# Optimization experiments

Hardware: AMD Instinct MI355X
Metric: run time of the kernel (lower is better)

## Reference

```python
import jax, jax.numpy as jnp
import numpy as np

B, S, H, I, E, K = 4, 2048, 1024, 4096, 8, 2


def setup_inputs() -> dict:
    key = jax.random.key(0)
    ks = jax.random.split(key, 5)
    scale = 1.0 / np.sqrt(H)
    return {
        "hidden_states": jax.random.normal(ks[0], (B, S, H), dtype=jnp.float32),
        "router_w": jax.random.normal(ks[1], (E, H), dtype=jnp.float32) * scale,
        "gate_w": jax.random.normal(ks[2], (E, I, H), dtype=jnp.float32) * scale,
        "up_w": jax.random.normal(ks[3], (E, I, H), dtype=jnp.float32) * scale,
        "down_w": jax.random.normal(ks[4], (E, H, I), dtype=jnp.float32) * (1.0 / np.sqrt(I)),
        "top_k": K,
    }


def reference(hidden_states, router_w, gate_w, up_w, down_w, top_k):
    # Router: logits -> softmax -> top-k -> renormalized weights (eval mode, no jitter)
    logits = jnp.einsum("bsh,eh->bse", hidden_states, router_w)
    probs = jax.nn.softmax(logits, axis=-1)
    expert_weights, expert_indices = jax.lax.top_k(probs, top_k)  # [B,S,K]
    expert_weights = expert_weights / expert_weights.sum(axis=-1, keepdims=True)

    n_experts = router_w.shape[0]
    # Per-token combine weight for each expert: [B,S,E]
    combine = (jax.nn.one_hot(expert_indices, n_experts, dtype=expert_weights.dtype)
               * expert_weights[..., None]).sum(axis=-2)

    out = jnp.zeros_like(hidden_states)
    for e in range(n_experts):  # fixed small expert count
        g = jax.nn.silu(hidden_states @ gate_w[e].T)  # [B,S,I]
        u = hidden_states @ up_w[e].T                 # [B,S,I]
        y = (g * u) @ down_w[e].T                     # [B,S,H]
        out = out + combine[..., e:e + 1] * y
    return out
```

## Files before the change

### kernel.cpp

```cpp
#include <hip/hip_runtime.h>
#include <hip/hip_bf16.h>
#include <math.h>
#include <stdint.h>

#define TOKENS 8192
#define HD 1024
#define ID 4096
#define NE 8
#define RMAX 18432
#define MAXT 72

typedef __attribute__((ext_vector_type(8))) short short8v;
typedef __attribute__((ext_vector_type(4))) float f32x4;

typedef const __attribute__((address_space(1))) unsigned int* gas_u32p;
typedef __attribute__((address_space(3))) unsigned int* las_u32p;

__device__ __forceinline__ void stage16(const void* g, void* l) {
  __builtin_amdgcn_global_load_lds((gas_u32p)g, (las_u32p)l, 16, 0, 0);
}

#define BARRIER asm volatile("s_barrier" ::: "memory")
#define WAITLGKM asm volatile("s_waitcnt lgkmcnt(0)" ::: "memory")
#define VMC0 asm volatile("s_waitcnt vmcnt(0)" ::: "memory")
#define VMC2 asm volatile("s_waitcnt vmcnt(2)" ::: "memory")
#define VMC6 asm volatile("s_waitcnt vmcnt(6)" ::: "memory")
#define VMC8 asm volatile("s_waitcnt vmcnt(8)" ::: "memory")

__global__ __launch_bounds__(256) void convert3_kernel(
    const float* __restrict__ s0, const float* __restrict__ s1, const float* __restrict__ s2,
    __hip_bfloat16* __restrict__ d0) {
  int r = blockIdx.x >> 14;
  const float* src = (r == 0) ? s0 : ((r == 1) ? s1 : s2);
  __hip_bfloat16* dst = d0 + (size_t)r * ((size_t)NE * ID * HD);
  size_t i = (((size_t)(blockIdx.x & 16383)) * 256 + threadIdx.x) * 8;
  float4 a = ((const float4*)(src + i))[0];
  float4 b = ((const float4*)(src + i))[1];
  union { __hip_bfloat16 h[8]; int4 v; } u;
  u.h[0] = __float2bfloat16(a.x); u.h[1] = __float2bfloat16(a.y);
  u.h[2] = __float2bfloat16(a.z); u.h[3] = __float2bfloat16(a.w);
  u.h[4] = __float2bfloat16(b.x); u.h[5] = __float2bfloat16(b.y);
  u.h[6] = __float2bfloat16(b.z); u.h[7] = __float2bfloat16(b.w);
  *(int4*)(dst + i) = u.v;
}

__global__ __launch_bounds__(256) void router_kernel(
    const float* __restrict__ h, const float* __restrict__ rw,
    __hip_bfloat16* __restrict__ hx, int* __restrict__ tidx,
    float* __restrict__ tw, int* __restrict__ cnt) {
  int wid = threadIdx.x >> 6, lane = threadIdx.x & 63;
  int t = blockIdx.x * 4 + wid;
  const float4* h4 = (const float4*)(h + (size_t)t * HD);
  float x[16];
  {
    float4 xa = h4[lane * 4 + 0], xb = h4[lane * 4 + 1], xc = h4[lane * 4 + 2], xd = h4[lane * 4 + 3];
    x[0] = xa.x; x[1] = xa.y; x[2] = xa.z; x[3] = xa.w;
    x[4] = xb.x; x[5] = xb.y; x[6] = xb.z; x[7] = xb.w;
    x[8] = xc.x; x[9] = xc.y; x[10] = xc.z; x[11] = xc.w;
    x[12] = xd.x; x[13] = xd.y; x[14] = xd.z; x[15] = xd.w;
  }
  union { __hip_bfloat16 hb[16]; int4 v[2]; } u;
#pragma unroll
  for (int j = 0; j < 16; j++) u.hb[j] = __float2bfloat16(x[j]);
  {
    int4* hxp = (int4*)(hx + (size_t)t * HD + lane * 16);
    hxp[0] = u.v[0]; hxp[1] = u.v[1];
  }
  double acc[NE];
#pragma unroll
  for (int e = 0; e < NE; e++) {
    const float4* w4 = (const float4*)(rw + e * HD);
    float4 wa = w4[lane * 4 + 0], wb = w4[lane * 4 + 1], wc = w4[lane * 4 + 2], wd = w4[lane * 4 + 3];
    double s = 0.0;
    s += (double)x[0] * wa.x + (double)x[1] * wa.y + (double)x[2] * wa.z + (double)x[3] * wa.w;
    s += (double)x[4] * wb.x + (double)x[5] * wb.y + (double)x[6] * wb.z + (double)x[7] * wb.w;
    s += (double)x[8] * wc.x + (double)x[9] * wc.y + (double)x[10] * wc.z + (double)x[11] * wc.w;
    s += (double)x[12] * wd.x + (double)x[13] * wd.y + (double)x[14] * wd.z + (double)x[15] * wd.w;
    acc[e] = s;
  }
#pragma unroll
  for (int off = 32; off >= 1; off >>= 1)
#pragma unroll
    for (int e = 0; e < NE; e++) acc[e] += __shfl_xor(acc[e], off, 64);
  if (lane == 0) {
    int i0 = 0; double l0 = acc[0];
#pragma unroll
    for (int e = 1; e < NE; e++) if (acc[e] > l0) { l0 = acc[e]; i0 = e; }
    int i1 = -1; double l1 = -1.0e300;
#pragma unroll
    for (int e = 0; e < NE; e++) if (e != i0 && acc[e] > l1) { l1 = acc[e]; i1 = e; }
    double r = exp(l1 - l0);
    float w0 = (float)(1.0 / (1.0 + r));
    float w1 = (float)(r / (1.0 + r));
    tidx[t * 2 + 0] = i0; tidx[t * 2 + 1] = i1;
    tw[t * 2 + 0] = w0;  tw[t * 2 + 1] = w1;
    atomicAdd(&cnt[i0], 1); atomicAdd(&cnt[i1], 1);
  }
}

__global__ void scan_kernel(const int* __restrict__ cnt, int* __restrict__ ofs, int* __restrict__ cnt2) {
  if (threadIdx.x == 0) {
    int a = 0;
    for (int e = 0; e < NE; e++) { ofs[e] = a; a += (cnt[e] + 255) & ~255; }
    ofs[NE] = a;
  }
  if (threadIdx.x < NE) cnt2[threadIdx.x] = 0;
}

__global__ __launch_bounds__(256) void scatter_kernel(
    const int* __restrict__ tidx, const float* __restrict__ tw,
    const int* __restrict__ ofs, int* __restrict__ cnt2,
    int* __restrict__ rowmap, int* __restrict__ slots) {
  int t = blockIdx.x * 256 + threadIdx.x;
#pragma unroll
  for (int k = 0; k < 2; k++) {
    int e = tidx[t * 2 + k];
    int pos = atomicAdd(&cnt2[e], 1);
    int row = ofs[e] + pos;
    rowmap[row] = t;
    slots[t * 2 + k] = row;
  }
}

#define MFMA44(ACC, AF, BF)                                                                \
  { _Pragma("unroll") for (int m_ = 0; m_ < 4; m_++)                                       \
    _Pragma("unroll") for (int n_ = 0; n_ < 4; n_++)                                       \
    _Pragma("unroll") for (int k_ = 0; k_ < 2; k_++)                                       \
      ACC[m_][n_] = __builtin_amdgcn_mfma_f32_16x16x32_bf16(                               \
          AF[m_][k_], BF[n_][k_], ACC[m_][n_], 0, 0, 0); }

__global__ __launch_bounds__(512, 2) void gemm1_kernel(
    const __hip_bfloat16* __restrict__ hx, const __hip_bfloat16* __restrict__ Wg,
    const __hip_bfloat16* __restrict__ Wu, const int* __restrict__ rowmap,
    const int* __restrict__ ofs, const __hip_bfloat16* __restrict__ zrow,
    __hip_bfloat16* __restrict__ act) {
  __shared__ __align__(128) char lds[131072];
  const int nwg = gridDim.x;
  int wg0 = blockIdx.x;
  int wg = (wg0 & 7) * (nwg >> 3) + (wg0 >> 3);
  const int tm = wg >> 5, tn = wg & 31;
  const int Rtot = ofs[NE];
  const int row0 = tm * 256;
  if (row0 >= Rtot) return;
  int e = 0;
#pragma unroll
  for (int i = 1; i < NE; i++) e += (row0 >= ofs[i]);
  const int tid = threadIdx.x, wid = tid >> 6, lane = tid & 63;
  const int wm = wid >> 1, wn = wid & 1;
  const int fr = lane & 15, fkE = (lane >> 4) << 3;
  const int wmB = wm * 64, wnB = wn * 64;

  const char* srcA[4]; const char* srcG[2]; const char* srcU[2];
  int ldA[4], ldG[2], ldU[2];
#pragma unroll
  for (int j = 0; j < 4; j++) {
    int d = j * 8192 + tid * 16;
    int row = d >> 7;
    int kb = (d ^ (((d >> 7) & 7) << 4)) & 127;
    int tok = rowmap[row0 + row];
    const __hip_bfloat16* base = (tok >= 0) ? (hx + (size_t)tok * HD) : zrow;
    srcA[j] = (const char*)base + kb;
    ldA[j] = j * 8192 + wid * 1024;
  }
#pragma unroll
  for (int j = 0; j < 2; j++) {
    int d = j * 8192 + tid * 16;
    int row = d >> 7;
    int kb = (d ^ (((d >> 7) & 7) << 4)) & 127;
    srcG[j] = (const char*)(Wg + ((size_t)e * ID + tn * 128 + row) * HD) + kb;
    srcU[j] = (const char*)(Wu + ((size_t)e * ID + tn * 128 + row) * HD) + kb;
    ldG[j] = 32768 + j * 8192 + wid * 1024;
    ldU[j] = 49152 + j * 8192 + wid * 1024;
  }
#define STG_A(j, t, bf) stage16(srcA[j] + (size_t)(t) * 128, (char*)lds + (bf) * 65536 + ldA[j])
#define STG_G(j, t, bf) stage16(srcG[j] + (size_t)(t) * 128, (char*)lds + (bf) * 65536 + ldG[j])
#define STG_U(j, t, bf) stage16(srcU[j] + (size_t)(t) * 128, (char*)lds + (bf) * 65536 + ldU[j])

  auto RD = [&](int bf, int poff, int rowi, int kki) -> short8v {
    int o = ((rowi + fr) << 7) + ((kki << 5) + fkE) * 2;
    o ^= ((o >> 7) & 7) << 4;
    return *(const short8v*)(&lds[bf * 65536 + poff + o]);
  };

  f32x4 accG[4][4], accU[4][4];
#pragma unroll
  for (int m = 0; m < 4; m++)
#pragma unroll
    for (int n = 0; n < 4; n++) { accG[m][n] = (f32x4)(0.0f); accU[m][n] = (f32x4)(0.0f); }

  const int NT = HD / 64;
#pragma unroll
  for (int j = 0; j < 4; j++) STG_A(j, 0, 0);
  STG_G(0, 0, 0); STG_G(1, 0, 0);
  STG_U(0, 0, 0); STG_U(1, 0, 0);
#pragma unroll
  for (int j = 0; j < 4; j++) STG_A(j, 1, 1);
  STG_G(0, 1, 1); STG_G(1, 1, 1);
  VMC8; BARRIER;

#pragma unroll 1
  for (int I = 0; I < NT / 2; ++I) {
    const int t0 = 2 * I;
    const bool more = (t0 + 2 < NT);
    short8v a[4][2], b[4][2];
#pragma unroll
    for (int m = 0; m < 4; m++) { a[m][0] = RD(0, 0, wmB + m * 16, 0); a[m][1] = RD(0, 0, wmB + m * 16, 1); }
#pragma unroll
    for (int n = 0; n < 4; n++) { b[n][0] = RD(0, 32768, wnB + n * 16, 0); b[n][1] = RD(0, 32768, wnB + n * 16, 1); }
    STG_U(0, t0 + 1, 1); STG_U(1, t0 + 1, 1);
    BARRIER; WAITLGKM;
    __builtin_amdgcn_s_setprio(1); MFMA44(accG, a, b); __builtin_amdgcn_s_setprio(0);
    VMC8; BARRIER;
#pragma unroll
    for (int n = 0; n < 4; n++) { b[n][0] = RD(0, 49152, wnB + n * 16, 0); b[n][1] = RD(0, 49152, wnB + n * 16, 1); }
    if (more) {
      STG_A(0, t0 + 2, 0); STG_A(1, t0 + 2, 0); STG_A(2, t0 + 2, 0); STG_A(3, t0 + 2, 0);
      STG_G(0, t0 + 2, 0); STG_G(1, t0 + 2, 0);
    }
    BARRIER; WAITLGKM;
    __builtin_amdgcn_s_setprio(1); MFMA44(accU, a, b); __builtin_amdgcn_s_setprio(0);
    if (more) { VMC8; } else { VMC2; }
    BARRIER;
#pragma unroll
    for (int m = 0; m < 4; m++) { a[m][0] = RD(1, 0, wmB + m * 16, 0); a[m][1] = RD(1, 0, wmB + m * 16, 1); }
#pragma unroll
    for (int n = 0; n < 4; n++) { b[n][0] = RD(1, 32768, wnB + n * 16, 0); b[n][1] = RD(1, 32768, wnB + n * 16, 1); }
    if (more) { STG_U(0, t0 + 2, 0); STG_U(1, t0 + 2, 0); }
    BARRIER; WAITLGKM;
    __builtin_amdgcn_s_setprio(1); MFMA44(accG, a, b); __builtin_amdgcn_s_setprio(0);
    if (more) { VMC8; } else { VMC0; }
    BARRIER;
#pragma unroll
    for (int n = 0; n < 4; n++) { b[n][0] = RD(1, 49152, wnB + n * 16, 0); b[n][1] = RD(1, 49152, wnB + n * 16, 1); }
    if (more) {
      STG_A(0, t0 + 3, 1); STG_A(1, t0 + 3, 1); STG_A(2, t0 + 3, 1); STG_A(3, t0 + 3, 1);
      STG_G(0, t0 + 3, 1); STG_G(1, t0 + 3, 1);
    }
    BARRIER; WAITLGKM;
    __builtin_amdgcn_s_setprio(1); MFMA44(accU, a, b); __builtin_amdgcn_s_setprio(0);
    if (more) { VMC8; } else { VMC0; }
    BARRIER;
  }
#undef STG_A
#undef STG_G
#undef STG_U

  const int rb = row0 + wmB + ((lane >> 4) << 2);
  const int cb = tn * 128 + wnB + fr;
#pragma unroll
  for (int m = 0; m < 4; m++)
#pragma unroll
    for (int i = 0; i < 4; i++) {
      int r = rb + m * 16 + i;
      __hip_bfloat16* dst = act + (size_t)r * ID + cb;
#pragma unroll
      for (int n = 0; n < 4; n++) {
        float g = accG[m][n][i], uu = accU[m][n][i];
        float s = g / (1.0f + __expf(-g));
        dst[n * 16] = __float2bfloat16(s * uu);
      }
    }
}

__global__ __launch_bounds__(512, 2) void gemm2_kernel(
    const __hip_bfloat16* __restrict__ act, const __hip_bfloat16* __restrict__ Wd,
    const int* __restrict__ ofs, float* __restrict__ ybuf) {
  __shared__ __align__(128) char lds[147456];
  const int nwg = gridDim.x;
  int wg0 = blockIdx.x;
  int wg = (wg0 & 7) * (nwg >> 3) + (wg0 >> 3);
  const int tm = wg >> 3, tn = wg & 7;
  const int Rtot = ofs[NE];
  const int row0 = tm * 256;
  if (row0 >= Rtot) return;
  int e = 0;
#pragma unroll
  for (int i = 1; i < NE; i++) e += (row0 >= ofs[i]);
  const int tid = threadIdx.x, wid = tid >> 6, lane = tid & 63;
  const int wm = wid >> 1, wn = wid & 1;
  const int fr = lane & 15, fkE = (lane >> 4) << 3;
  const int wmB = wm * 64, wnB = wn * 64;

  const char* srcA[4]; const char* srcB[2];
  int ldA[4], ldB[2];
#pragma unroll
  for (int j = 0; j < 4; j++) {
    int d = j * 8192 + tid * 16;
    int row = d >> 7;
    int kb = (d ^ (((d >> 7) & 7) << 4)) & 127;
    srcA[j] = (const char*)(act + (size_t)(row0 + row) * ID) + kb;
    ldA[j] = j * 8192 + wid * 1024;
  }
#pragma unroll
  for (int j = 0; j < 2; j++) {
    int d = j * 8192 + tid * 16;
    int row = d >> 7;
    int kb = (d ^ (((d >> 7) & 7) << 4)) & 127;
    srcB[j] = (const char*)(Wd + ((size_t)e * HD + tn * 128 + row) * ID) + kb;
    ldB[j] = 32768 + j * 8192 + wid * 1024;
  }
#define STG_A2(j, t, q) stage16(srcA[j] + (size_t)(t) * 128, (char*)lds + (q) * 49152 + ldA[j])
#define STG_B2(j, t, q) stage16(srcB[j] + (size_t)(t) * 128, (char*)lds + (q) * 49152 + ldB[j])

  auto RD = [&](const char* base, int poff, int rowi, int kki) -> short8v {
    int o = ((rowi + fr) << 7) + ((kki << 5) + fkE) * 2;
    o ^= ((o >> 7) & 7) << 4;
    return *(const short8v*)(base + poff + o);
  };

  f32x4 acc[4][4];
#pragma unroll
  for (int m = 0; m < 4; m++)
#pragma unroll
    for (int n = 0; n < 4; n++) acc[m][n] = (f32x4)(0.0f);

  const int NT = ID / 64;
#pragma unroll
  for (int j = 0; j < 4; j++) STG_A2(j, 0, 0);
  STG_B2(0, 0, 0); STG_B2(1, 0, 0);
#pragma unroll
  for (int j = 0; j < 4; j++) STG_A2(j, 1, 1);
  STG_B2(0, 1, 1); STG_B2(1, 1, 1);
  VMC6; BARRIER;

  int bq = 0;
#pragma unroll 1
  for (int T = 0; T < NT; ++T) {
    const bool more = (T + 2 < NT);
    int sq = (bq >= 1) ? (bq - 1) : 2;
    const char* base = (const char*)lds + bq * 49152;
    short8v a[4][2], b[4][2];
#pragma unroll
    for (int m = 0; m < 4; m++) { a[m][0] = RD(base, 0, wmB + m * 16, 0); a[m][1] = RD(base, 0, wmB + m * 16, 1); }
#pragma unroll
    for (int n = 0; n < 4; n++) { b[n][0] = RD(base, 32768, wnB + n * 16, 0); b[n][1] = RD(base, 32768, wnB + n * 16, 1); }
    if (more) {
      STG_A2(0, T + 2, sq); STG_A2(1, T + 2, sq); STG_A2(2, T + 2, sq); STG_A2(3, T + 2, sq);
      STG_B2(0, T + 2, sq); STG_B2(1, T + 2, sq);
    }
    BARRIER; WAITLGKM;
    __builtin_amdgcn_s_setprio(1); MFMA44(acc, a, b); __builtin_amdgcn_s_setprio(0);
    if (more) { VMC6; } else { VMC0; }
    BARRIER;
    bq = (bq == 2) ? 0 : (bq + 1);
  }
#undef STG_A2
#undef STG_B2

  const int rb = row0 + wmB + ((lane >> 4) << 2);
  const int cb = tn * 128 + wnB + fr;
#pragma unroll
  for (int m = 0; m < 4; m++)
#pragma unroll
    for (int i = 0; i < 4; i++) {
      int r = rb + m * 16 + i;
      float* dst = ybuf + (size_t)r * HD + cb;
#pragma unroll
      for (int n = 0; n < 4; n++) dst[n * 16] = acc[m][n][i];
    }
}

__global__ __launch_bounds__(256) void combine_kernel(
    const float* __restrict__ ybuf, const int* __restrict__ slots,
    const float* __restrict__ tw, float* __restrict__ out) {
  int t = blockIdx.x * 4 + (threadIdx.x >> 6);
  int lane = threadIdx.x & 63;
  int r0 = slots[t * 2 + 0], r1 = slots[t * 2 + 1];
  float w0 = tw[t * 2 + 0], w1 = tw[t * 2 + 1];
  const float4* y0 = (const float4*)(ybuf + (size_t)r0 * HD);
  const float4* y1 = (const float4*)(ybuf + (size_t)r1 * HD);
  float4* o = (float4*)(out + (size_t)t * HD);
#pragma unroll
  for (int j = 0; j < 4; j++) {
    int ix = j * 64 + lane;
    float4 a = y0[ix], b = y1[ix];
    float4 c;
    c.x = w0 * a.x + w1 * b.x; c.y = w0 * a.y + w1 * b.y;
    c.z = w0 * a.z + w1 * b.z; c.w = w0 * a.w + w1 * b.w;
    o[ix] = c;
  }
}

extern "C" void kernel_launch(void* const* d_in, const int* in_sizes, int n_in,
                              void* d_out, int out_size, void* d_ws, size_t ws_size,
                              hipStream_t stream) {
  (void)in_sizes; (void)n_in; (void)out_size; (void)ws_size;
  const float* h  = (const float*)d_in[0];
  const float* rw = (const float*)d_in[1];
  const float* gw = (const float*)d_in[2];
  const float* uw = (const float*)d_in[3];
  const float* dw = (const float*)d_in[4];
  float* out = (float*)d_out;

  char* ws = (char*)d_ws;
  size_t off = 0;
  auto alloc = [&](size_t bytes) { char* p = ws + off; off += (bytes + 255) & ~255ULL; return p; };
  __hip_bfloat16* wg  = (__hip_bfloat16*)alloc((size_t)NE * ID * HD * 2);
  __hip_bfloat16* wu  = (__hip_bfloat16*)alloc((size_t)NE * ID * HD * 2);
  __hip_bfloat16* wd  = (__hip_bfloat16*)alloc((size_t)NE * HD * ID * 2);
  __hip_bfloat16* act = (__hip_bfloat16*)alloc((size_t)RMAX * ID * 2);
  __hip_bfloat16* hx  = (__hip_bfloat16*)alloc((size_t)TOKENS * HD * 2);
  float* ybuf = (float*)alloc((size_t)RMAX * HD * 4);
  __hip_bfloat16* zrow = (__hip_bfloat16*)alloc(HD * 2);
  int* rowmap = (int*)alloc(RMAX * 4);
  int* tidx   = (int*)alloc(TOKENS * 2 * 4);
  float* twt  = (float*)alloc(TOKENS * 2 * 4);
  int* slots  = (int*)alloc(TOKENS * 2 * 4);
  int* cnt    = (int*)alloc(256);
  int* cnt2   = (int*)alloc(256);
  int* ofs    = (int*)alloc(256);

  hipMemsetAsync(cnt, 0, NE * 4, stream);
  hipMemsetAsync(rowmap, 0xFF, RMAX * 4, stream);
  hipMemsetAsync(zrow, 0, HD * 2, stream);

  convert3_kernel<<<49152, 256, 0, stream>>>(gw, uw, dw, wg);
  router_kernel<<<TOKENS / 4, 256, 0, stream>>>(h, rw, hx, tidx, twt, cnt);
  scan_kernel<<<1, 64, 0, stream>>>(cnt, ofs, cnt2);
  scatter_kernel<<<TOKENS / 256, 256, 0, stream>>>(tidx, twt, ofs, cnt2, rowmap, slots);
  gemm1_kernel<<<MAXT * 32, 512, 0, stream>>>(hx, wg, wu, rowmap, ofs, zrow, act);
  gemm2_kernel<<<MAXT * 8, 512, 0, stream>>>(act, wd, ofs, ybuf);
  combine_kernel<<<TOKENS / 4, 256, 0, stream>>>(ybuf, slots, twt, out);
}
```

Baseline: 919.2 us.

## Enlarge GEMM warp tiles to 128x64, fuse combine into gemm2 via atomics

Both expert GEMMs move to a 4x2 wave layout where each wave computes a 128x64 tile over an 8-phase K loop. Gemm1 stacks the gate and up weights into one 256-wide B tile and pairs the G and U halves through LDS in the epilogue. Gemm2 widens its N tile to 256 and scatters weighted results directly into the output with float atomics, which removes the ybuf round trip and the combine kernel. This costs a memset of the output, atomic contention on each token's two expert rows, and more accumulator registers per wave.

Result: slower. 1.097 ms (+19.3%).

```diff
diff --git a/kernel.cpp b/kernel.cpp
--- a/kernel.cpp
+++ b/kernel.cpp
@@ -23,9 +23,7 @@
 #define BARRIER asm volatile("s_barrier" ::: "memory")
 #define WAITLGKM asm volatile("s_waitcnt lgkmcnt(0)" ::: "memory")
 #define VMC0 asm volatile("s_waitcnt vmcnt(0)" ::: "memory")
-#define VMC2 asm volatile("s_waitcnt vmcnt(2)" ::: "memory")
-#define VMC6 asm volatile("s_waitcnt vmcnt(6)" ::: "memory")
-#define VMC8 asm volatile("s_waitcnt vmcnt(8)" ::: "memory")
+#define VMC4 asm volatile("s_waitcnt vmcnt(4)" ::: "memory")
 
 __global__ __launch_bounds__(256) void convert3_kernel(
     const float* __restrict__ s0, const float* __restrict__ s1, const float* __restrict__ s2,
@@ -110,7 +108,7 @@
 __global__ __launch_bounds__(256) void scatter_kernel(
     const int* __restrict__ tidx, const float* __restrict__ tw,
     const int* __restrict__ ofs, int* __restrict__ cnt2,
-    int* __restrict__ rowmap, int* __restrict__ slots) {
+    int* __restrict__ rowmap, float* __restrict__ wrow) {
   int t = blockIdx.x * 256 + threadIdx.x;
 #pragma unroll
   for (int k = 0; k < 2; k++) {
@@ -118,16 +116,77 @@
     int pos = atomicAdd(&cnt2[e], 1);
     int row = ofs[e] + pos;
     rowmap[row] = t;
-    slots[t * 2 + k] = row;
-  }
-}
-
-#define MFMA44(ACC, AF, BF)                                                                \
+    wrow[row] = tw[t * 2 + k];
+  }
+}
+
+#define MFMA16(ACC, MO, AF, BF)                                                            \
   { _Pragma("unroll") for (int m_ = 0; m_ < 4; m_++)                                       \
     _Pragma("unroll") for (int n_ = 0; n_ < 4; n_++)                                       \
-    _Pragma("unroll") for (int k_ = 0; k_ < 2; k_++)                                       \
-      ACC[m_][n_] = __builtin_amdgcn_mfma_f32_16x16x32_bf16(                               \
-          AF[m_][k_], BF[n_][k_], ACC[m_][n_], 0, 0, 0); }
+      ACC[(MO) + m_][n_] = __builtin_amdgcn_mfma_f32_16x16x32_bf16(                        \
+          AF[m_], BF[n_], ACC[(MO) + m_][n_], 0, 0, 0); }
+
+#define KLOOP_8PHASE(NT)                                                                   \
+  _Pragma("unroll 1")                                                                      \
+  for (int I = 0; I < (NT) / 2; ++I) {                                                     \
+    const int t0 = 2 * I;                                                                  \
+    const bool more = (t0 + 2 < (NT));                                                     \
+    short8v a0[4], a1[4], b0[4], b1[4];                                                    \
+                                                                                   \
+    _Pragma("unroll") for (int m = 0; m < 4; m++) a0[m] = RD(0, 0, wmB + m * 16, 0);       \
+    _Pragma("unroll") for (int n = 0; n < 4; n++) b0[n] = RD(0, 32768, wnB + n * 16, 0);   \
+    STG_A(0, t0 + 1, 1); STG_A(1, t0 + 1, 1);                                              \
+    BARRIER; WAITLGKM;                                                                     \
+    __builtin_amdgcn_s_setprio(1); MFMA16(acc, 0, a0, b0); __builtin_amdgcn_s_setprio(0);  \
+    BARRIER;                                                                               \
+                                                                                   \
+    _Pragma("unroll") for (int m = 0; m < 4; m++) a1[m] = RD(0, 0, wmB + m * 16, 1);       \
+    _Pragma("unroll") for (int n = 0; n < 4; n++) b1[n] = RD(0, 32768, wnB + n * 16, 1);   \
+    STG_A(2, t0 + 1, 1); STG_A(3, t0 + 1, 1);                                              \
+    BARRIER; WAITLGKM;                                                                     \
+    __builtin_amdgcn_s_setprio(1); MFMA16(acc, 0, a1, b1); __builtin_amdgcn_s_setprio(0);  \
+    BARRIER;                                                                               \
+                                                                                   \
+    _Pragma("unroll") for (int m = 0; m < 4; m++) a0[m] = RD(0, 0, wmB + 64 + m * 16, 0);  \
+    if (more) { STG_B(0, t0 + 2, 0); STG_B(1, t0 + 2, 0); }                                \
+    BARRIER; WAITLGKM;                                                                     \
+    __builtin_amdgcn_s_setprio(1); MFMA16(acc, 4, a0, b0); __builtin_amdgcn_s_setprio(0);  \
+    BARRIER;                                                                               \
+                                                                                   \
+    _Pragma("unroll") for (int m = 0; m < 4; m++) a1[m] = RD(0, 0, wmB + 64 + m * 16, 1);  \
+    if (more) { STG_B(2, t0 + 2, 0); STG_B(3, t0 + 2, 0); }                                \
+    BARRIER; WAITLGKM;                                                                     \
+    __builtin_amdgcn_s_setprio(1); MFMA16(acc, 4, a1, b1); __builtin_amdgcn_s_setprio(0);  \
+    if (more) { VMC4; } else { VMC0; }                                                     \
+    BARRIER;                                                                               \
+                                                                                   \
+    _Pragma("unroll") for (int m = 0; m < 4; m++) a0[m] = RD(1, 0, wmB + m * 16, 0);       \
+    _Pragma("unroll") for (int n = 0; n < 4; n++) b0[n] = RD(1, 32768, wnB + n * 16, 0);   \
+    if (more) { STG_A(0, t0 + 2, 0); STG_A(1, t0 + 2, 0); }                                \
+    BARRIER; WAITLGKM;                                                                     \
+    __builtin_amdgcn_s_setprio(1); MFMA16(acc, 0, a0, b0); __builtin_amdgcn_s_setprio(0);  \
+    BARRIER;                                                                               \
+                                                                                   \
+    _Pragma("unroll") for (int m = 0; m < 4; m++) a1[m] = RD(1, 0, wmB + m * 16, 1);       \
+    _Pragma("unroll") for (int n = 0; n < 4; n++) b1[n] = RD(1, 32768, wnB + n * 16, 1);   \
+    if (more) { STG_A(2, t0 + 2, 0); STG_A(3, t0 + 2, 0); }                                \
+    BARRIER; WAITLGKM;                                                                     \
+    __builtin_amdgcn_s_setprio(1); MFMA16(acc, 0, a1, b1); __builtin_amdgcn_s_setprio(0);  \
+    BARRIER;                                                                               \
+                                                                                   \
+    _Pragma("unroll") for (int m = 0; m < 4; m++) a0[m] = RD(1, 0, wmB + 64 + m * 16, 0);  \
+    if (more) { STG_B(0, t0 + 3, 1); STG_B(1, t0 + 3, 1); }                                \
+    BARRIER; WAITLGKM;                                                                     \
+    __builtin_amdgcn_s_setprio(1); MFMA16(acc, 4, a0, b0); __builtin_amdgcn_s_setprio(0);  \
+    BARRIER;                                                                               \
+                                                                                   \
+    _Pragma("unroll") for (int m = 0; m < 4; m++) a1[m] = RD(1, 0, wmB + 64 + m * 16, 1);  \
+    if (more) { STG_B(2, t0 + 3, 1); STG_B(3, t0 + 3, 1); }                                \
+    BARRIER; WAITLGKM;                                                                     \
+    __builtin_amdgcn_s_setprio(1); MFMA16(acc, 4, a1, b1); __builtin_amdgcn_s_setprio(0);  \
+    if (more) { VMC4; } else { VMC0; }                                                     \
+    BARRIER;                                                                               \
+  }
 
 __global__ __launch_bounds__(512, 2) void gemm1_kernel(
     const __hip_bfloat16* __restrict__ hx, const __hip_bfloat16* __restrict__ Wg,
@@ -146,35 +205,29 @@
 #pragma unroll
   for (int i = 1; i < NE; i++) e += (row0 >= ofs[i]);
   const int tid = threadIdx.x, wid = tid >> 6, lane = tid & 63;
-  const int wm = wid >> 1, wn = wid & 1;
+  const int wm = wid >> 2, wn = wid & 3;
   const int fr = lane & 15, fkE = (lane >> 4) << 3;
-  const int wmB = wm * 64, wnB = wn * 64;
-
-  const char* srcA[4]; const char* srcG[2]; const char* srcU[2];
-  int ldA[4], ldG[2], ldU[2];
+  const int wmB = wm * 128, wnB = wn * 64;
+
+  const char* srcA[4]; const char* srcB[4];
+  int ldA[4], ldB[4];
 #pragma unroll
   for (int j = 0; j < 4; j++) {
     int d = j * 8192 + tid * 16;
     int row = d >> 7;
     int kb = (d ^ (((d >> 7) & 7) << 4)) & 127;
     int tok = rowmap[row0 + row];
-    const __hip_bfloat16* base = (tok >= 0) ? (hx + (size_t)tok * HD) : zrow;
-    srcA[j] = (const char*)base + kb;
+    const __hip_bfloat16* abase = (tok >= 0) ? (hx + (size_t)tok * HD) : zrow;
+    srcA[j] = (const char*)abase + kb;
     ldA[j] = j * 8192 + wid * 1024;
-  }
-#pragma unroll
-  for (int j = 0; j < 2; j++) {
-    int d = j * 8192 + tid * 16;
-    int row = d >> 7;
-    int kb = (d ^ (((d >> 7) & 7) << 4)) & 127;
-    srcG[j] = (const char*)(Wg + ((size_t)e * ID + tn * 128 + row) * HD) + kb;
-    srcU[j] = (const char*)(Wu + ((size_t)e * ID + tn * 128 + row) * HD) + kb;
-    ldG[j] = 32768 + j * 8192 + wid * 1024;
-    ldU[j] = 49152 + j * 8192 + wid * 1024;
+    const __hip_bfloat16* wbase = (row < 128)
+        ? (Wg + ((size_t)e * ID + tn * 128 + row) * HD)
+        : (Wu + ((size_t)e * ID + tn * 128 + (row - 128)) * HD);
+    srcB[j] = (const char*)wbase + kb;
+    ldB[j] = 32768 + j * 8192 + wid * 1024;
   }
 #define STG_A(j, t, bf) stage16(srcA[j] + (size_t)(t) * 128, (char*)lds + (bf) * 65536 + ldA[j])
-#define STG_G(j, t, bf) stage16(srcG[j] + (size_t)(t) * 128, (char*)lds + (bf) * 65536 + ldG[j])
-#define STG_U(j, t, bf) stage16(srcU[j] + (size_t)(t) * 128, (char*)lds + (bf) * 65536 + ldU[j])
+#define STG_B(j, t, bf) stage16(srcB[j] + (size_t)(t) * 128, (char*)lds + (bf) * 65536 + ldB[j])
 
   auto RD = [&](int bf, int poff, int rowi, int kki) -> short8v {
     int o = ((rowi + fr) << 7) + ((kki << 5) + fkE) * 2;
@@ -182,94 +235,62 @@
     return *(const short8v*)(&lds[bf * 65536 + poff + o]);
   };
 
-  f32x4 accG[4][4], accU[4][4];
+  f32x4 acc[8][4];
+#pragma unroll
+  for (int m = 0; m < 8; m++)
+#pragma unroll
+    for (int n = 0; n < 4; n++) acc[m][n] = (f32x4)(0.0f);
+
+  const int NT = HD / 64;
+#pragma unroll
+  for (int j = 0; j < 4; j++) STG_A(j, 0, 0);
+#pragma unroll
+  for (int j = 0; j < 4; j++) STG_B(j, 0, 0);
+#pragma unroll
+  for (int j = 0; j < 4; j++) STG_B(j, 1, 1);
+  VMC4; BARRIER;
+
+  KLOOP_8PHASE(NT)
+#undef STG_A
+#undef STG_B
+
+  const bool isG = (wn < 2);
+  float* xslot = (float*)(lds + wid * 16384);
+  const float* pslot = (const float*)(lds + (wid ^ 2) * 16384);
 #pragma unroll
   for (int m = 0; m < 4; m++)
 #pragma unroll
-    for (int n = 0; n < 4; n++) { accG[m][n] = (f32x4)(0.0f); accU[m][n] = (f32x4)(0.0f); }
-
-  const int NT = HD / 64;
-#pragma unroll
-  for (int j = 0; j < 4; j++) STG_A(j, 0, 0);
-  STG_G(0, 0, 0); STG_G(1, 0, 0);
-  STG_U(0, 0, 0); STG_U(1, 0, 0);
-#pragma unroll
-  for (int j = 0; j < 4; j++) STG_A(j, 1, 1);
-  STG_G(0, 1, 1); STG_G(1, 1, 1);
-  VMC8; BARRIER;
-
-#pragma unroll 1
-  for (int I = 0; I < NT / 2; ++I) {
-    const int t0 = 2 * I;
-    const bool more = (t0 + 2 < NT);
-    short8v a[4][2], b[4][2];
-#pragma unroll
-    for (int m = 0; m < 4; m++) { a[m][0] = RD(0, 0, wmB + m * 16, 0); a[m][1] = RD(0, 0, wmB + m * 16, 1); }
-#pragma unroll
-    for (int n = 0; n < 4; n++) { b[n][0] = RD(0, 32768, wnB + n * 16, 0); b[n][1] = RD(0, 32768, wnB + n * 16, 1); }
-    STG_U(0, t0 + 1, 1); STG_U(1, t0 + 1, 1);
-    BARRIER; WAITLGKM;
-    __builtin_amdgcn_s_setprio(1); MFMA44(accG, a, b); __builtin_amdgcn_s_setprio(0);
-    VMC8; BARRIER;
-#pragma unroll
-    for (int n = 0; n < 4; n++) { b[n][0] = RD(0, 49152, wnB + n * 16, 0); b[n][1] = RD(0, 49152, wnB + n * 16, 1); }
-    if (more) {
-      STG_A(0, t0 + 2, 0); STG_A(1, t0 + 2, 0); STG_A(2, t0 + 2, 0); STG_A(3, t0 + 2, 0);
-      STG_G(0, t0 + 2, 0); STG_G(1, t0 + 2, 0);
-    }
-    BARRIER; WAITLGKM;
-    __builtin_amdgcn_s_setprio(1); MFMA44(accU, a, b); __builtin_amdgcn_s_setprio(0);
-    if (more) { VMC8; } else { VMC2; }
-    BARRIER;
-#pragma unroll
-    for (int m = 0; m < 4; m++) { a[m][0] = RD(1, 0, wmB + m * 16, 0); a[m][1] = RD(1, 0, wmB + m * 16, 1); }
-#pragma unroll
-    for (int n = 0; n < 4; n++) { b[n][0] = RD(1, 32768, wnB + n * 16, 0); b[n][1] = RD(1, 32768, wnB + n * 16, 1); }
-    if (more) { STG_U(0, t0 + 2, 0); STG_U(1, t0 + 2, 0); }
-    BARRIER; WAITLGKM;
-    __builtin_amdgcn_s_setprio(1); MFMA44(accG, a, b); __builtin_amdgcn_s_setprio(0);
-    if (more) { VMC8; } else { VMC0; }
-    BARRIER;
-#pragma unroll
-    for (int n = 0; n < 4; n++) { b[n][0] = RD(1, 49152, wnB + n * 16, 0); b[n][1] = RD(1, 49152, wnB + n * 16, 1); }
-    if (more) {
-      STG_A(0, t0 + 3, 1); STG_A(1, t0 + 3, 1); STG_A(2, t0 + 3, 1); STG_A(3, t0 + 3, 1);
-      STG_G(0, t0 + 3, 1); STG_G(1, t0 + 3, 1);
-    }
-    BARRIER; WAITLGKM;
-    __builtin_amdgcn_s_setprio(1); MFMA44(accU, a, b); __builtin_amdgcn_s_setprio(0);
-    if (more) { VMC8; } else { VMC0; }
-    BARRIER;
-  }
-#undef STG_A
-#undef STG_G
-#undef STG_U
-
-  const int rb = row0 + wmB + ((lane >> 4) << 2);
-  const int cb = tn * 128 + wnB + fr;
+    for (int n = 0; n < 4; n++)
+      *(f32x4*)(xslot + (size_t)(m * 4 + n) * 256 + lane * 4) = acc[isG ? 4 + m : m][n];
+  __syncthreads();
+  const int g4 = (lane >> 4) << 2;
+  const int colb = tn * 128 + (wn & 1) * 64 + fr;
+  const int rb = row0 + wmB + (isG ? 0 : 64) + g4;
 #pragma unroll
   for (int m = 0; m < 4; m++)
 #pragma unroll
-    for (int i = 0; i < 4; i++) {
-      int r = rb + m * 16 + i;
-      __hip_bfloat16* dst = act + (size_t)r * ID + cb;
-#pragma unroll
-      for (int n = 0; n < 4; n++) {
-        float g = accG[m][n][i], uu = accU[m][n][i];
+    for (int n = 0; n < 4; n++) {
+      f32x4 other = *(const f32x4*)(pslot + (size_t)(m * 4 + n) * 256 + lane * 4);
+      f32x4 own = acc[isG ? m : 4 + m][n];
+#pragma unroll
+      for (int i = 0; i < 4; i++) {
+        float g = isG ? own[i] : other[i];
+        float u = isG ? other[i] : own[i];
         float s = g / (1.0f + __expf(-g));
-        dst[n * 16] = __float2bfloat16(s * uu);
+        act[(size_t)(rb + m * 16 + i) * ID + colb + n * 16] = __float2bfloat16(s * u);
       }
     }
 }
 
 __global__ __launch_bounds__(512, 2) void gemm2_kernel(
     const __hip_bfloat16* __restrict__ act, const __hip_bfloat16* __restrict__ Wd,
-    const int* __restrict__ ofs, float* __restrict__ ybuf) {
-  __shared__ __align__(128) char lds[147456];
+    const int* __restrict__ rowmap, const float* __restrict__ wrow,
+    const int* __restrict__ ofs, float* __restrict__ out) {
+  __shared__ __align__(128) char lds[131072];
   const int nwg = gridDim.x;
   int wg0 = blockIdx.x;
   int wg = (wg0 & 7) * (nwg >> 3) + (wg0 >> 3);
-  const int tm = wg >> 3, tn = wg & 7;
+  const int tm = wg >> 2, tn = wg & 3;
   const int Rtot = ofs[NE];
   const int row0 = tm * 256;
   if (row0 >= Rtot) return;
@@ -277,12 +298,12 @@
 #pragma unroll
   for (int i = 1; i < NE; i++) e += (row0 >= ofs[i]);
   const int tid = threadIdx.x, wid = tid >> 6, lane = tid & 63;
-  const int wm = wid >> 1, wn = wid & 1;
+  const int wm = wid >> 2, wn = wid & 3;
   const int fr = lane & 15, fkE = (lane >> 4) << 3;
-  const int wmB = wm * 64, wnB = wn * 64;
-
-  const char* srcA[4]; const char* srcB[2];
-  int ldA[4], ldB[2];
+  const int wmB = wm * 128, wnB = wn * 64;
+
+  const char* srcA[4]; const char* srcB[4];
+  int ldA[4], ldB[4];
 #pragma unroll
   for (int j = 0; j < 4; j++) {
     int d = j * 8192 + tid * 16;
@@ -290,101 +311,60 @@
     int kb = (d ^ (((d >> 7) & 7) << 4)) & 127;
     srcA[j] = (const char*)(act + (size_t)(row0 + row) * ID) + kb;
     ldA[j] = j * 8192 + wid * 1024;
-  }
-#pragma unroll
-  for (int j = 0; j < 2; j++) {
-    int d = j * 8192 + tid * 16;
-    int row = d >> 7;
-    int kb = (d ^ (((d >> 7) & 7) << 4)) & 127;
-    srcB[j] = (const char*)(Wd + ((size_t)e * HD + tn * 128 + row) * ID) + kb;
+    srcB[j] = (const char*)(Wd + ((size_t)e * HD + tn * 256 + row) * ID) + kb;
     ldB[j] = 32768 + j * 8192 + wid * 1024;
   }
-#define STG_A2(j, t, q) stage16(srcA[j] + (size_t)(t) * 128, (char*)lds + (q) * 49152 + ldA[j])
-#define STG_B2(j, t, q) stage16(srcB[j] + (size_t)(t) * 128, (char*)lds + (q) * 49152 + ldB[j])
-
-  auto RD = [&](const char* base, int poff, int rowi, int kki) -> short8v {
+#define STG_A(j, t, bf) stage16(srcA[j] + (size_t)(t) * 128, (char*)lds + (bf) * 65536 + ldA[j])
+#define STG_B(j, t, bf) stage16(srcB[j] + (size_t)(t) * 128, (char*)lds + (bf) * 65536 + ldB[j])
+
+  auto RD = [&](int bf, int poff, int rowi, int kki) -> short8v {
     int o = ((rowi + fr) << 7) + ((kki << 5) + fkE) * 2;
     o ^= ((o >> 7) & 7) << 4;
-    return *(const short8v*)(base + poff + o);
+    return *(const short8v*)(&lds[bf * 65536 + poff + o]);
   };
 
-  f32x4 acc[4][4];
-#pragma unroll
-  for (int m = 0; m < 4; m++)
+  f32x4 acc[8][4];
+#pragma unroll
+  for (int m = 0; m < 8; m++)
 #pragma unroll
     for (int n = 0; n < 4; n++) acc[m][n] = (f32x4)(0.0f);
 
   const int NT = ID / 64;
 #pragma unroll
-  for (int j = 0; j < 4; j++) STG_A2(j, 0, 0);
-  STG_B2(0, 0, 0); STG_B2(1, 0, 0);
-#pragma unroll
-  for (int j = 0; j < 4; j++) STG_A2(j, 1, 1);
-  STG_B2(0, 1, 1); STG_B2(1, 1, 1);
-  VMC6; BARRIER;
-
-  int bq = 0;
-#pragma unroll 1
-  for (int T = 0; T < NT; ++T) {
-    const bool more = (T + 2 < NT);
-    int sq = (bq >= 1) ? (bq - 1) : 2;
-    const char* base = (const char*)lds + bq * 49152;
-    short8v a[4][2], b[4][2];
-#pragma unroll
-    for (int m = 0; m < 4; m++) { a[m][0] = RD(base, 0, wmB + m * 16, 0); a[m][1] = RD(base, 0, wmB + m * 16, 1); }
-#pragma unroll
-    for (int n = 0; n < 4; n++) { b[n][0] = RD(base, 32768, wnB + n * 16, 0); b[n][1] = RD(base, 32768, wnB + n * 16, 1); }
-    if (more) {
-      STG_A2(0, T + 2, sq); STG_A2(1, T + 2, sq); STG_A2(2, T + 2, sq); STG_A2(3, T + 2, sq);
-      STG_B2(0, T + 2, sq); STG_B2(1, T + 2, sq);
+  for (int j = 0; j < 4; j++) STG_A(j, 0, 0);
+#pragma unroll
+  for (int j = 0; j < 4; j++) STG_B(j, 0, 0);
+#pragma unroll
+  for (int j = 0; j < 4; j++) STG_B(j, 1, 1);
+  VMC4; BARRIER;
+
+  KLOOP_8PHASE(NT)
+#undef STG_A
+#undef STG_B
+
+  const int g4 = (lane >> 4) << 2;
+  const int colb = tn * 256 + wnB + fr;
+#pragma unroll
+  for (int m = 0; m < 8; m++) {
+    const int rbase = row0 + wmB + m * 16 + g4;
+#pragma unroll
+    for (int i = 0; i < 4; i++) {
+      int rr = rbase + i;
+      int tok = rowmap[rr];
+      if (tok >= 0) {
+        float w = wrow[rr];
+        float* dst = out + (size_t)tok * HD + colb;
+#pragma unroll
+        for (int n = 0; n < 4; n++) atomicAdd(dst + n * 16, w * acc[m][n][i]);
+      }
     }
-    BARRIER; WAITLGKM;
-    __builtin_amdgcn_s_setprio(1); MFMA44(acc, a, b); __builtin_amdgcn_s_setprio(0);
-    if (more) { VMC6; } else { VMC0; }
-    BARRIER;
-    bq = (bq == 2) ? 0 : (bq + 1);
-  }
-#undef STG_A2
-#undef STG_B2
-
-  const int rb = row0 + wmB + ((lane >> 4) << 2);
-  const int cb = tn * 128 + wnB + fr;
-#pragma unroll
-  for (int m = 0; m < 4; m++)
-#pragma unroll
-    for (int i = 0; i < 4; i++) {
-      int r = rb + m * 16 + i;
-      float* dst = ybuf + (size_t)r * HD + cb;
-#pragma unroll
-      for (int n = 0; n < 4; n++) dst[n * 16] = acc[m][n][i];
-    }
-}
-
-__global__ __launch_bounds__(256) void combine_kernel(
-    const float* __restrict__ ybuf, const int* __restrict__ slots,
-    const float* __restrict__ tw, float* __restrict__ out) {
-  int t = blockIdx.x * 4 + (threadIdx.x >> 6);
-  int lane = threadIdx.x & 63;
-  int r0 = slots[t * 2 + 0], r1 = slots[t * 2 + 1];
-  float w0 = tw[t * 2 + 0], w1 = tw[t * 2 + 1];
-  const float4* y0 = (const float4*)(ybuf + (size_t)r0 * HD);
-  const float4* y1 = (const float4*)(ybuf + (size_t)r1 * HD);
-  float4* o = (float4*)(out + (size_t)t * HD);
-#pragma unroll
-  for (int j = 0; j < 4; j++) {
-    int ix = j * 64 + lane;
-    float4 a = y0[ix], b = y1[ix];
-    float4 c;
-    c.x = w0 * a.x + w1 * b.x; c.y = w0 * a.y + w1 * b.y;
-    c.z = w0 * a.z + w1 * b.z; c.w = w0 * a.w + w1 * b.w;
-    o[ix] = c;
   }
 }
 
 extern "C" void kernel_launch(void* const* d_in, const int* in_sizes, int n_in,
                               void* d_out, int out_size, void* d_ws, size_t ws_size,
                               hipStream_t stream) {
-  (void)in_sizes; (void)n_in; (void)out_size; (void)ws_size;
+  (void)in_sizes; (void)n_in; (void)ws_size;
   const float* h  = (const float*)d_in[0];
   const float* rw = (const float*)d_in[1];
   const float* gw = (const float*)d_in[2];
@@ -400,12 +380,11 @@
   __hip_bfloat16* wd  = (__hip_bfloat16*)alloc((size_t)NE * HD * ID * 2);
   __hip_bfloat16* act = (__hip_bfloat16*)alloc((size_t)RMAX * ID * 2);
   __hip_bfloat16* hx  = (__hip_bfloat16*)alloc((size_t)TOKENS * HD * 2);
-  float* ybuf = (float*)alloc((size_t)RMAX * HD * 4);
   __hip_bfloat16* zrow = (__hip_bfloat16*)alloc(HD * 2);
   int* rowmap = (int*)alloc(RMAX * 4);
+  float* wrow = (float*)alloc(RMAX * 4);
   int* tidx   = (int*)alloc(TOKENS * 2 * 4);
   float* twt  = (float*)alloc(TOKENS * 2 * 4);
-  int* slots  = (int*)alloc(TOKENS * 2 * 4);
   int* cnt    = (int*)alloc(256);
   int* cnt2   = (int*)alloc(256);
   int* ofs    = (int*)alloc(256);
@@ -413,12 +392,12 @@
   hipMemsetAsync(cnt, 0, NE * 4, stream);
   hipMemsetAsync(rowmap, 0xFF, RMAX * 4, stream);
   hipMemsetAsync(zrow, 0, HD * 2, stream);
+  hipMemsetAsync(out, 0, (size_t)out_size * 4, stream);
 
   convert3_kernel<<<49152, 256, 0, stream>>>(gw, uw, dw, wg);
   router_kernel<<<TOKENS / 4, 256, 0, stream>>>(h, rw, hx, tidx, twt, cnt);
   scan_kernel<<<1, 64, 0, stream>>>(cnt, ofs, cnt2);
-  scatter_kernel<<<TOKENS / 256, 256, 0, stream>>>(tidx, twt, ofs, cnt2, rowmap, slots);
+  scatter_kernel<<<TOKENS / 256, 256, 0, stream>>>(tidx, twt, ofs, cnt2, rowmap, wrow);
   gemm1_kernel<<<MAXT * 32, 512, 0, stream>>>(hx, wg, wu, rowmap, ofs, zrow, act);
-  gemm2_kernel<<<MAXT * 8, 512, 0, stream>>>(act, wd, ofs, ybuf);
-  combine_kernel<<<TOKENS / 4, 256, 0, stream>>>(ybuf, slots, twt, out);
-}
+  gemm2_kernel<<<MAXT * 4, 512, 0, stream>>>(act, wd, rowmap, wrow, ofs, out);
+}
```
